# Kernel optimization log

Hardware: AMD Instinct MI355X
Metric: run time of the kernel (lower is better)

Reference implementation:

```python
import jax, jax.numpy as jnp
import numpy as np

N_USERS = 100000
N_ITEMS = 50000
N_NODES = N_USERS + N_ITEMS
DIM = 64
N_EDGES = 1200000
BATCH = 4096


def _propagate(edge_index, emb):
    # row = source, col = destination (out[dst] += norm * emb[src])
    row, col = edge_index[0], edge_index[1]
    n = emb.shape[0]
    # degree counted over row occurrences only (faithful to `degree(row, ...)`)
    deg = jax.ops.segment_sum(jnp.ones_like(row, dtype=emb.dtype), row, num_segments=n)
    dinv = jnp.where(deg > 0, deg ** -0.5, 0.0).astype(emb.dtype)
    norm = dinv[row] * dinv[col]  # [E]
    msgs = norm[:, None] * emb[row]  # [E, D] gather + scale
    return jax.ops.segment_sum(msgs, col, num_segments=n)  # scatter-add into dst


def setup_inputs() -> dict:
    key = jax.random.key(0)
    ks = jax.random.split(key, 10)
    xavier = (6.0 / (N_USERS + DIM)) ** 0.5  # approximate xavier bounds per table
    user_emb = jax.random.uniform(ks[0], (N_USERS, DIM), jnp.float32, -xavier, xavier)
    xavier_i = (6.0 / (N_ITEMS + DIM)) ** 0.5
    item_emb = jax.random.uniform(ks[1], (N_ITEMS, DIM), jnp.float32, -xavier_i, xavier_i)
    lim = (1.0 / DIM) ** 0.5
    W1 = jax.random.uniform(ks[2], (DIM, DIM), jnp.float32, -lim, lim)
    b1 = jax.random.uniform(ks[3], (DIM,), jnp.float32, -lim, lim)
    W2 = jax.random.uniform(ks[4], (DIM, DIM), jnp.float32, -lim, lim)
    b2 = jax.random.uniform(ks[5], (DIM,), jnp.float32, -lim, lim)
    users = jax.random.randint(ks[6], (BATCH,), 0, N_USERS)
    items = jax.random.randint(ks[7], (BATCH,), 0, N_ITEMS)
    edge_index = jax.random.randint(ks[8], (2, N_EDGES), 0, N_NODES)
    return {"users": users, "items": items, "edge_index": edge_index,
            "user_emb": user_emb, "item_emb": item_emb,
            "W1": W1, "b1": b1, "W2": W2, "b2": b2}


def reference(users, items, edge_index, user_emb, item_emb, W1, b1, W2, b2):
    all_emb = jnp.concatenate([user_emb, item_emb], axis=0)  # [N, D]
    # layer 0: propagate -> linear -> relu
    all_emb = _propagate(edge_index, all_emb)
    all_emb = jax.nn.relu(all_emb @ W1.T + b1)
    # layer 1 (last): propagate -> linear (no relu)
    all_emb = _propagate(edge_index, all_emb)
    all_emb = all_emb @ W2.T + b2
    user_final = all_emb[:N_USERS]
    item_final = all_emb[N_USERS:]
    scores = jnp.sum(user_final[users] * item_final[items], axis=1)  # [B]
    return scores
```

## Files before the change

kernel.cpp:

```cpp
#include <hip/hip_runtime.h>
#include <math.h>

constexpr int NU = 100000;
constexpr int NI = 50000;
constexpr int NN = 150000;
constexpr int D  = 64;
constexpr int NE = 1200000;
constexpr int NE4 = NE / 4;
constexpr int B  = 4096;
constexpr int CAPB = 64;
constexpr int CAP2 = 40;

constexpr int NCHUNK = 3;
constexpr int CHUNK  = 65536;
constexpr int CWORDS = CHUNK / 4;
constexpr int WORDS  = 37504;
constexpr int RWORDS = 37500;
constexpr int NSLICE = 80;
constexpr int SLICE4 = NE4 / NSLICE;


__global__ void k_flag(const int* __restrict__ users, const int* __restrict__ items,
                       int* flags, int* __restrict__ bidx, int* __restrict__ nb) {
    const int t = blockIdx.x * blockDim.x + threadIdx.x;
    if (t >= 2 * B) return;
    const int node = (t < B) ? users[t] : items[t - B] + NU;
    const int old = atomicOr(&flags[node], 1);
    if (!(old & 1)) bidx[node] = atomicAdd(nb, 1);
}

__global__ void __launch_bounds__(256) k_hist(const int* __restrict__ row,
                                              unsigned int* __restrict__ hcopy) {
    __shared__ unsigned int lh[CWORDS];
    const int ci = blockIdx.x / NSLICE;
    const int si = blockIdx.x % NSLICE;
    const int lo = ci * CHUNK;
    const int cw = (ci == NCHUNK - 1) ? (WORDS - (NCHUNK - 1) * CWORDS) : CWORDS;
    for (int w = threadIdx.x; w < cw; w += 256) lh[w] = 0;
    __syncthreads();
    const int4* r4 = reinterpret_cast<const int4*>(row) + (size_t)si * SLICE4;
    const unsigned int span = (unsigned)(cw * 4);
    for (int t = threadIdx.x; t < SLICE4; t += 256) {
        const int4 r = r4[t];
        int v;
        v = r.x - lo; if ((unsigned)v < span) atomicAdd(&lh[v >> 2], 1u << (8 * (v & 3)));
        v = r.y - lo; if ((unsigned)v < span) atomicAdd(&lh[v >> 2], 1u << (8 * (v & 3)));
        v = r.z - lo; if ((unsigned)v < span) atomicAdd(&lh[v >> 2], 1u << (8 * (v & 3)));
        v = r.w - lo; if ((unsigned)v < span) atomicAdd(&lh[v >> 2], 1u << (8 * (v & 3)));
    }
    __syncthreads();
    unsigned int* dst = hcopy + (size_t)si * WORDS + ci * CWORDS;
    for (int w = threadIdx.x; w < cw; w += 256) dst[w] = lh[w];
}

__global__ void k_mark(const int* __restrict__ row, const int* __restrict__ col,
                       const int* __restrict__ bidx,
                       int* __restrict__ cntBd, int* __restrict__ csrBd, int* flags) {
    const int t = blockIdx.x * blockDim.x + threadIdx.x;
    if (t >= NE4) return;
    const int4 r = reinterpret_cast<const int4*>(row)[t];
    const int4 c = reinterpret_cast<const int4*>(col)[t];
    #define E1(rr, cc) if (flags[cc] & 1) { \
        const int bi = bidx[cc]; \
        const int s = atomicAdd(&cntBd[bi], 1); \
        csrBd[bi * CAPB + s] = rr; \
        flags[rr] |= 2; }
    E1(r.x, c.x) E1(r.y, c.y) E1(r.z, c.z) E1(r.w, c.w)
    #undef E1
}

__global__ void k_dinvc(const unsigned int* __restrict__ hcopy,
                        float* __restrict__ dinv, const int* __restrict__ flags,
                        int* __restrict__ list, int* __restrict__ ncnt) {
    const int w = blockIdx.x * blockDim.x + threadIdx.x;
    if (w >= RWORDS) return;
    unsigned int s = 0;
    #pragma unroll 8
    for (int si = 0; si < NSLICE; ++si) s += hcopy[(size_t)si * WORDS + w];
    const int d0 = s & 255, d1 = (s >> 8) & 255, d2 = (s >> 16) & 255, d3 = (int)(s >> 24);
    float4 dv;
    dv.x = d0 > 0 ? 1.0f / sqrtf((float)d0) : 0.0f;
    dv.y = d1 > 0 ? 1.0f / sqrtf((float)d1) : 0.0f;
    dv.z = d2 > 0 ? 1.0f / sqrtf((float)d2) : 0.0f;
    dv.w = d3 > 0 ? 1.0f / sqrtf((float)d3) : 0.0f;
    reinterpret_cast<float4*>(dinv)[w] = dv;
    const int4 fl = reinterpret_cast<const int4*>(flags)[w];
    const int n0 = w * 4;
    if (fl.x & 2) list[atomicAdd(ncnt, 1)] = n0;
    if (fl.y & 2) list[atomicAdd(ncnt, 1)] = n0 + 1;
    if (fl.z & 2) list[atomicAdd(ncnt, 1)] = n0 + 2;
    if (fl.w & 2) list[atomicAdd(ncnt, 1)] = n0 + 3;
}

__global__ void k_pass2(const int* __restrict__ row, const int* __restrict__ col,
                        const int* __restrict__ flags,
                        int* __restrict__ cnt2d, int* __restrict__ csr2d) {
    const int t = blockIdx.x * blockDim.x + threadIdx.x;
    if (t >= NE4) return;
    const int4 r = reinterpret_cast<const int4*>(row)[t];
    const int4 c = reinterpret_cast<const int4*>(col)[t];
    #define E2(rr, cc) if (flags[cc] & 2) { \
        const int s = atomicAdd(&cnt2d[cc], 1); \
        csr2d[cc * CAP2 + s] = rr; }
    E2(r.x, c.x) E2(r.y, c.y) E2(r.z, c.z) E2(r.w, c.w)
    #undef E2
}

__global__ void k_gather1(const int* __restrict__ list, const int* __restrict__ ncnt,
                          const int* __restrict__ cnt2d, const int* __restrict__ csr2d,
                          const float* __restrict__ dinv,
                          const float* __restrict__ embU, const float* __restrict__ embI,
                          float* __restrict__ out) {
    const int lane = threadIdx.x & 63;
    const int idx = blockIdx.x * (blockDim.x >> 6) + (threadIdx.x >> 6);
    if (idx >= *ncnt) return;
    const int c = list[idx];
    const int n = cnt2d[c];
    const int* es = csr2d + (size_t)c * CAP2;
    float acc = 0.0f;
    int e = 0;
    for (; e + 1 < n; e += 2) {
        const int r0 = es[e], r1 = es[e + 1];
        const float d0 = dinv[r0], d1 = dinv[r1];
        const float* s0 = (r0 < NU) ? embU + (size_t)r0 * D : embI + (size_t)(r0 - NU) * D;
        const float* s1 = (r1 < NU) ? embU + (size_t)r1 * D : embI + (size_t)(r1 - NU) * D;
        const float v0 = s0[lane], v1 = s1[lane];
        acc = fmaf(d0, v0, acc);
        acc = fmaf(d1, v1, acc);
    }
    if (e < n) {
        const int r = es[e];
        const float* s = (r < NU) ? embU + (size_t)r * D : embI + (size_t)(r - NU) * D;
        acc = fmaf(dinv[r], s[lane], acc);
    }
    out[(size_t)c * D + lane] = dinv[c] * acc;
}

__global__ void __launch_bounds__(256) k_mlp_relu(const int* __restrict__ list,
                                                  const int* __restrict__ ncnt,
                                                  float* __restrict__ emb,
                                                  const float* __restrict__ W,
                                                  const float* __restrict__ b) {
    const int lane = threadIdx.x & 63;
    float w[D];
    #pragma unroll
    for (int k4 = 0; k4 < D / 4; ++k4) {
        const float4 v = *reinterpret_cast<const float4*>(W + (size_t)lane * D + k4 * 4);
        w[k4 * 4 + 0] = v.x; w[k4 * 4 + 1] = v.y;
        w[k4 * 4 + 2] = v.z; w[k4 * 4 + 3] = v.w;
    }
    const float bias = b[lane];

    const int n = *ncnt;
    const int wid = blockIdx.x * (blockDim.x >> 6) + (threadIdx.x >> 6);
    const int nw  = gridDim.x * (blockDim.x >> 6);
    for (int i4 = wid * 4; i4 < n; i4 += nw * 4) {
        const int r0 = list[i4];
        const int r1 = (i4 + 1 < n) ? list[i4 + 1] : r0;
        const int r2 = (i4 + 2 < n) ? list[i4 + 2] : r0;
        const int r3 = (i4 + 3 < n) ? list[i4 + 3] : r0;
        float* x0 = emb + (size_t)r0 * D;
        float* x1 = emb + (size_t)r1 * D;
        float* x2 = emb + (size_t)r2 * D;
        float* x3 = emb + (size_t)r3 * D;
        const float xv0 = x0[lane], xv1 = x1[lane], xv2 = x2[lane], xv3 = x3[lane];
        float a0 = bias, a1 = bias, a2 = bias, a3 = bias;
        #pragma unroll
        for (int k = 0; k < D; ++k) {
            const float wk = w[k];
            a0 = fmaf(__int_as_float(__builtin_amdgcn_readlane(__float_as_int(xv0), k)), wk, a0);
            a1 = fmaf(__int_as_float(__builtin_amdgcn_readlane(__float_as_int(xv1), k)), wk, a1);
            a2 = fmaf(__int_as_float(__builtin_amdgcn_readlane(__float_as_int(xv2), k)), wk, a2);
            a3 = fmaf(__int_as_float(__builtin_amdgcn_readlane(__float_as_int(xv3), k)), wk, a3);
        }
        x0[lane] = fmaxf(a0, 0.0f);
        x1[lane] = fmaxf(a1, 0.0f);
        x2[lane] = fmaxf(a2, 0.0f);
        x3[lane] = fmaxf(a3, 0.0f);
    }
}

__global__ void k_score2(const int* __restrict__ users, const int* __restrict__ items,
                         const int* __restrict__ bidx, const int* __restrict__ cntBd,
                         const int* __restrict__ csrBd,
                         const float* __restrict__ dinv, const float* __restrict__ embA,
                         const float* __restrict__ W, const float* __restrict__ b,
                         float* __restrict__ out) {
    __shared__ float sWt[D * D];
    __shared__ float sb[D];
    __shared__ float sx[4][D];
    for (int i = threadIdx.x; i < D * D; i += blockDim.x)
        sWt[i] = W[(size_t)(i & 63) * D + (i >> 6)];
    if (threadIdx.x < D) sb[threadIdx.x] = b[threadIdx.x];
    __syncthreads();
    const int lane = threadIdx.x & 63;
    const int wid  = threadIdx.x >> 6;
    const int p = blockIdx.x * (blockDim.x >> 6) + wid;
    if (p >= B) return;

    float y[2];
    const int node[2] = { users[p], items[p] + NU };
    #pragma unroll
    for (int t = 0; t < 2; ++t) {
        const int c = node[t];
        const int bi = bidx[c];
        const int n = cntBd[bi];
        const int* es = csrBd + (size_t)bi * CAPB;
        float acc = 0.0f;
        for (int e = 0; e < n; ++e) {
            const int r = es[e];
            acc = fmaf(dinv[r], embA[(size_t)r * D + lane], acc);
        }
        sx[wid][lane] = dinv[c] * acc;
        float yv = sb[lane];
        #pragma unroll
        for (int k = 0; k < D; ++k)
            yv = fmaf(sx[wid][k], sWt[k * D + lane], yv);
        y[t] = yv;
    }
    float prod = y[0] * y[1];
    #pragma unroll
    for (int off = 32; off >= 1; off >>= 1) prod += __shfl_down(prod, off, 64);
    if (lane == 0) out[p] = prod;
}

extern "C" void kernel_launch(void* const* d_in, const int* in_sizes, int n_in,
                              void* d_out, int out_size, void* d_ws, size_t ws_size,
                              hipStream_t stream) {
    const int*   users    = (const int*)d_in[0];
    const int*   items    = (const int*)d_in[1];
    const int*   edge     = (const int*)d_in[2];
    const float* user_emb = (const float*)d_in[3];
    const float* item_emb = (const float*)d_in[4];
    const float* W1       = (const float*)d_in[5];
    const float* b1       = (const float*)d_in[6];
    const float* W2       = (const float*)d_in[7];
    const float* b2       = (const float*)d_in[8];
    float*       out      = (float*)d_out;

    const int* row  = edge;
    const int* colp = edge + NE;

    int*   flags = (int*)d_ws;
    int*   cnt2d = (int*)d_ws + 150016;
    int*   cntBd = (int*)d_ws + 300032;
    int*   nb    = (int*)d_ws + 308480;
    int*   ncnt  = (int*)d_ws + 308496;
    float* dinv  = (float*)d_ws + 308512;
    int*   bidx  = (int*)d_ws + 458528;
    int*   list  = (int*)d_ws + 608544;
    int*   csrBd = (int*)d_ws + 758560;
    int*   csr2d = (int*)d_ws + 1299232;
    float* embA  = (float*)d_ws + 7299872;
    unsigned int* hcopy = (unsigned int*)csr2d;

    hipMemsetAsync(flags, 0, (size_t)308512 * sizeof(int), stream);

    k_flag <<<(2 * B + 255) / 256, 256, 0, stream>>>(users, items, flags, bidx, nb);
    k_hist <<<NCHUNK * NSLICE, 256, 0, stream>>>(row, hcopy);
    k_mark <<<(NE4 + 255) / 256, 256, 0, stream>>>(row, colp, bidx, cntBd, csrBd, flags);
    k_dinvc<<<(RWORDS + 255) / 256, 256, 0, stream>>>(hcopy, dinv, flags, list, ncnt);
    k_pass2<<<(NE4 + 255) / 256, 256, 0, stream>>>(row, colp, flags, cnt2d, csr2d);

    k_gather1 <<<(NN + 3) / 4, 256, 0, stream>>>(list, ncnt, cnt2d, csr2d, dinv,
                                                 user_emb, item_emb, embA);
    k_mlp_relu<<<2048, 256, 0, stream>>>(list, ncnt, embA, W1, b1);
    k_score2<<<B / 4, 256, 0, stream>>>(users, items, bidx, cntBd, csrBd, dinv, embA,
                                        W2, b2, out);
}
```

Measured before the change: 182.5 us.

## Fuse layer-1 neighbor gather with MLP+ReLU into one persistent kernel

Merges the gather kernel and the separate MLP/ReLU kernel into one grid-stride kernel. Each wavefront aggregates a node's neighbors into a register and immediately applies W1 (transposed into shared memory) plus bias and ReLU before a single store. The neighbor loop now reads four CSR indices at once with an int4 load and keeps four independent accumulators. This removes one launch and the write-then-reread of the intermediate embeddings. In exchange, every block reloads W1 into LDS, and the matvec now reads weights from LDS instead of registers.

```diff
diff --git a/kernel.cpp b/kernel.cpp
--- a/kernel.cpp
+++ b/kernel.cpp
@@ -106,77 +106,57 @@
     #undef E2
 }
 
-__global__ void k_gather1(const int* __restrict__ list, const int* __restrict__ ncnt,
-                          const int* __restrict__ cnt2d, const int* __restrict__ csr2d,
-                          const float* __restrict__ dinv,
-                          const float* __restrict__ embU, const float* __restrict__ embI,
-                          float* __restrict__ out) {
+__global__ void __launch_bounds__(256) k_gmlp(const int* __restrict__ list,
+                                              const int* __restrict__ ncnt,
+                                              const int* __restrict__ cnt2d,
+                                              const int* __restrict__ csr2d,
+                                              const float* __restrict__ dinv,
+                                              const float* __restrict__ embU,
+                                              const float* __restrict__ embI,
+                                              const float* __restrict__ W,
+                                              const float* __restrict__ b,
+                                              float* __restrict__ emb) {
+    __shared__ float sWt[D * D];
+    __shared__ float sb[D];
+    for (int i = threadIdx.x; i < D * D; i += blockDim.x)
+        sWt[i] = W[(size_t)(i & 63) * D + (i >> 6)];
+    if (threadIdx.x < D) sb[threadIdx.x] = b[threadIdx.x];
+    __syncthreads();
+
     const int lane = threadIdx.x & 63;
-    const int idx = blockIdx.x * (blockDim.x >> 6) + (threadIdx.x >> 6);
-    if (idx >= *ncnt) return;
-    const int c = list[idx];
-    const int n = cnt2d[c];
-    const int* es = csr2d + (size_t)c * CAP2;
-    float acc = 0.0f;
-    int e = 0;
-    for (; e + 1 < n; e += 2) {
-        const int r0 = es[e], r1 = es[e + 1];
-        const float d0 = dinv[r0], d1 = dinv[r1];
-        const float* s0 = (r0 < NU) ? embU + (size_t)r0 * D : embI + (size_t)(r0 - NU) * D;
-        const float* s1 = (r1 < NU) ? embU + (size_t)r1 * D : embI + (size_t)(r1 - NU) * D;
-        const float v0 = s0[lane], v1 = s1[lane];
-        acc = fmaf(d0, v0, acc);
-        acc = fmaf(d1, v1, acc);
-    }
-    if (e < n) {
-        const int r = es[e];
-        const float* s = (r < NU) ? embU + (size_t)r * D : embI + (size_t)(r - NU) * D;
-        acc = fmaf(dinv[r], s[lane], acc);
-    }
-    out[(size_t)c * D + lane] = dinv[c] * acc;
-}
-
-__global__ void __launch_bounds__(256) k_mlp_relu(const int* __restrict__ list,
-                                                  const int* __restrict__ ncnt,
-                                                  float* __restrict__ emb,
-                                                  const float* __restrict__ W,
-                                                  const float* __restrict__ b) {
-    const int lane = threadIdx.x & 63;
-    float w[D];
-    #pragma unroll
-    for (int k4 = 0; k4 < D / 4; ++k4) {
-        const float4 v = *reinterpret_cast<const float4*>(W + (size_t)lane * D + k4 * 4);
-        w[k4 * 4 + 0] = v.x; w[k4 * 4 + 1] = v.y;
-        w[k4 * 4 + 2] = v.z; w[k4 * 4 + 3] = v.w;
-    }
-    const float bias = b[lane];
-
     const int n = *ncnt;
-    const int wid = blockIdx.x * (blockDim.x >> 6) + (threadIdx.x >> 6);
-    const int nw  = gridDim.x * (blockDim.x >> 6);
-    for (int i4 = wid * 4; i4 < n; i4 += nw * 4) {
-        const int r0 = list[i4];
-        const int r1 = (i4 + 1 < n) ? list[i4 + 1] : r0;
-        const int r2 = (i4 + 2 < n) ? list[i4 + 2] : r0;
-        const int r3 = (i4 + 3 < n) ? list[i4 + 3] : r0;
-        float* x0 = emb + (size_t)r0 * D;
-        float* x1 = emb + (size_t)r1 * D;
-        float* x2 = emb + (size_t)r2 * D;
-        float* x3 = emb + (size_t)r3 * D;
-        const float xv0 = x0[lane], xv1 = x1[lane], xv2 = x2[lane], xv3 = x3[lane];
-        float a0 = bias, a1 = bias, a2 = bias, a3 = bias;
+    const int nwv = gridDim.x * (blockDim.x >> 6);
+    for (int idx = blockIdx.x * (blockDim.x >> 6) + (threadIdx.x >> 6);
+         idx < n; idx += nwv) {
+        const int c = list[idx];
+        const int ne = cnt2d[c];
+        const int* es = csr2d + (size_t)c * CAP2;
+        float a0 = 0.0f, a1 = 0.0f, a2 = 0.0f, a3 = 0.0f;
+        int e = 0;
+        for (; e + 3 < ne; e += 4) {
+            const int4 r = *reinterpret_cast<const int4*>(es + e);
+            const float d0 = dinv[r.x], d1 = dinv[r.y], d2 = dinv[r.z], d3 = dinv[r.w];
+            const float* s0 = (r.x < NU) ? embU + (size_t)r.x * D : embI + (size_t)(r.x - NU) * D;
+            const float* s1 = (r.y < NU) ? embU + (size_t)r.y * D : embI + (size_t)(r.y - NU) * D;
+            const float* s2 = (r.z < NU) ? embU + (size_t)r.z * D : embI + (size_t)(r.z - NU) * D;
+            const float* s3 = (r.w < NU) ? embU + (size_t)r.w * D : embI + (size_t)(r.w - NU) * D;
+            a0 = fmaf(d0, s0[lane], a0);
+            a1 = fmaf(d1, s1[lane], a1);
+            a2 = fmaf(d2, s2[lane], a2);
+            a3 = fmaf(d3, s3[lane], a3);
+        }
+        for (; e < ne; ++e) {
+            const int r = es[e];
+            const float* s = (r < NU) ? embU + (size_t)r * D : embI + (size_t)(r - NU) * D;
+            a0 = fmaf(dinv[r], s[lane], a0);
+        }
+        const float x = dinv[c] * ((a0 + a1) + (a2 + a3));
+        float y = sb[lane];
         #pragma unroll
-        for (int k = 0; k < D; ++k) {
-            const float wk = w[k];
-            a0 = fmaf(__int_as_float(__builtin_amdgcn_readlane(__float_as_int(xv0), k)), wk, a0);
-            a1 = fmaf(__int_as_float(__builtin_amdgcn_readlane(__float_as_int(xv1), k)), wk, a1);
-            a2 = fmaf(__int_as_float(__builtin_amdgcn_readlane(__float_as_int(xv2), k)), wk, a2);
-            a3 = fmaf(__int_as_float(__builtin_amdgcn_readlane(__float_as_int(xv3), k)), wk, a3);
-        }
-        x0[lane] = fmaxf(a0, 0.0f);
-        x1[lane] = fmaxf(a1, 0.0f);
-        x2[lane] = fmaxf(a2, 0.0f);
-        x3[lane] = fmaxf(a3, 0.0f);
+        for (int k = 0; k < D; ++k)
+            y = fmaf(__int_as_float(__builtin_amdgcn_readlane(__float_as_int(x), k)),
+                     sWt[k * D + lane], y);
+        emb[(size_t)c * D + lane] = fmaxf(y, 0.0f);
     }
 }
 
@@ -262,9 +242,8 @@
     k_dinvc<<<(RWORDS + 255) / 256, 256, 0, stream>>>(hcopy, dinv, flags, list, ncnt);
     k_pass2<<<(NE4 + 255) / 256, 256, 0, stream>>>(row, colp, flags, cnt2d, csr2d);
 
-    k_gather1 <<<(NN + 3) / 4, 256, 0, stream>>>(list, ncnt, cnt2d, csr2d, dinv,
-                                                 user_emb, item_emb, embA);
-    k_mlp_relu<<<2048, 256, 0, stream>>>(list, ncnt, embA, W1, b1);
+    k_gmlp <<<2560, 256, 0, stream>>>(list, ncnt, cnt2d, csr2d, dinv,
+                                      user_emb, item_emb, W1, b1, embA);
     k_score2<<<B / 4, 256, 0, stream>>>(users, items, bidx, cntBd, csrBd, dinv, embA,
                                         W2, b2, out);
 }
```

After: 194.1 us. +6.4%, slower.
